# Performance work log

Measured on AMD Instinct MI355X. Metric: run time of the kernel, lower is better.

The kernel has to match this reference:

```python
import jax, jax.numpy as jnp
import numpy as np

NEMBEDS = 512
EMBED_DIM = 64


def setup_inputs() -> dict:
    key = jax.random.key(0)
    k1, k2 = jax.random.split(key)
    z_e = jax.random.normal(k1, (32, EMBED_DIM, 64, 64), dtype=jnp.float32)
    codebook = jax.random.uniform(
        k2, (NEMBEDS, EMBED_DIM), dtype=jnp.float32,
        minval=-1.0 / NEMBEDS, maxval=1.0 / NEMBEDS)
    return {"z_e": z_e, "codebook": codebook}


def reference(z_e, codebook):
    # NCHW -> NHWC, flatten spatial+batch into tokens
    z = jnp.transpose(z_e, (0, 2, 3, 1))          # [B,H,W,D]
    B, H, W, D = z.shape
    flat = z.reshape(-1, D)                        # [N,D]
    # squared L2 distances (argmin of ||.||_2 == argmin of ||.||_2^2)
    # expanded form avoids the [N,K,D] broadcast intermediate
    d2 = (jnp.sum(flat * flat, axis=-1, keepdims=True)
          - 2.0 * flat @ codebook.T
          + jnp.sum(codebook * codebook, axis=-1))  # [N,K]
    inds = jnp.argmin(d2, axis=1)                   # [N]
    # direct gather == one-hot matmul lookup
    z_q = codebook[inds].reshape(B, H, W, D)        # [B,H,W,D]
    # commitment + codebook loss, per-batch mean over H,W,D
    sg = jax.lax.stop_gradient
    vq_loss = (jnp.mean((sg(z) - z_q) ** 2, axis=(1, 2, 3))
               + 0.25 * jnp.mean((z - sg(z_q)) ** 2, axis=(1, 2, 3)))  # [B]
    # straight-through estimator
    z_q_st = z + sg(z_q - z)
    out = jnp.transpose(z_q_st, (0, 3, 1, 2))       # back to NCHW
    return out, vq_loss, inds[:, None]
```

## Files before the change

kernel.cpp:

```cpp
#include <hip/hip_runtime.h>

#define NEMB 512
#define DIM 64
#define NB 32
#define HW 4096
#define NTOK (NB * HW)
#define TPB 256
#define TOKBLK 256
#define BLOCKS (NTOK / TOKBLK)

typedef float f32x16 __attribute__((ext_vector_type(16)));
typedef short bf16x8 __attribute__((ext_vector_type(8)));

#define WS_PART 0
#define WS_SUMC 512
#define WS_CMAXP 1024
#define WS_SCMAXP 1032
#define WS_CH 1040

__device__ __forceinline__ unsigned short f2bf(float f) {
    unsigned u = __float_as_uint(f);
    unsigned r = u + 0x7FFFu + ((u >> 16) & 1u);
    return (unsigned short)(r >> 16);
}

__global__ void vq_prep(const float* __restrict__ cb, float* __restrict__ ws)
{
    const int tid = threadIdx.x;
    const int k   = blockIdx.x * 64 + tid;

    float sc_v;
    {
#pragma clang fp contract(off)
        float s = 0.f;
#pragma unroll
        for (int d = 0; d < DIM; ++d) {
            float v = cb[k * DIM + d];
            float p = v * v;
            s = s + p;
        }
        sc_v = s;
        ws[WS_SUMC + k] = s;
    }

    float cmax_t = 0.f;
    uint4* chf = (uint4*)(ws + WS_CH);
    const int ct  = k >> 5;
    const int col = k & 31;
#pragma unroll
    for (int bd = 0; bd < 8; ++bd) {
        unsigned wd[4];
#pragma unroll
        for (int q = 0; q < 4; ++q) {
            float v0 = cb[k * DIM + 8 * bd + 2 * q];
            float v1 = cb[k * DIM + 8 * bd + 2 * q + 1];
            cmax_t = fmaxf(cmax_t, fmaxf(fabsf(v0), fabsf(v1)));
            wd[q] = (unsigned)f2bf(v0) | ((unsigned)f2bf(v1) << 16);
        }
        chf[(ct * 8 + bd) * 32 + col] = make_uint4(wd[0], wd[1], wd[2], wd[3]);
    }

    float cm = cmax_t, sm = sc_v;
#pragma unroll
    for (int off = 32; off; off >>= 1) {
        cm = fmaxf(cm, __shfl_xor(cm, off));
        sm = fmaxf(sm, __shfl_xor(sm, off));
    }
    if (tid == 0) {
        ws[WS_CMAXP  + blockIdx.x] = cm;
        ws[WS_SCMAXP + blockIdx.x] = sm;
    }
}

__global__ __launch_bounds__(TPB, 2)
void vq_main(const float* __restrict__ z_e, const float* __restrict__ cb,
             const float* __restrict__ ws, float* __restrict__ out,
             float* __restrict__ loss_part, float* __restrict__ inds_out)
{
    __shared__ float sumc_s[NEMB];
    __shared__ float red_s[TPB];
    __shared__ float sc2[2];

    const int tid  = threadIdx.x;
    const int gid  = blockIdx.x;
    const int b    = gid >> 4;
    const int base = (gid & 15) * TOKBLK;
    const int l    = tid & 63;
    const int col  = l & 31;
    const int half = l >> 5;

    sumc_s[tid]       = ws[WS_SUMC + tid];
    sumc_s[tid + TPB] = ws[WS_SUMC + tid + TPB];
    if (tid == 0) {
        float cm = ws[WS_CMAXP], sm = ws[WS_SCMAXP];
#pragma unroll
        for (int i = 1; i < 8; ++i) {
            cm = fmaxf(cm, ws[WS_CMAXP + i]);
            sm = fmaxf(sm, ws[WS_SCMAXP + i]);
        }
        sc2[0] = cm; sc2[1] = sm;
    }

    const float* zb = z_e + (size_t)b * DIM * HW;
    const int hwme = base + tid;
    float z[DIM];
    float sumz;
    {
#pragma clang fp contract(off)
        sumz = 0.f;
#pragma unroll
        for (int d = 0; d < DIM; ++d) {
            float v = zb[(size_t)d * HW + hwme];
            z[d] = v;
            float p = v * v;
            sumz = sumz + p;
        }
    }
    float l1own = 0.f, szown = 0.f;
#pragma unroll
    for (int d = 0; d < DIM; ++d) {
        l1own += fabsf(z[d]);
        szown = fmaf(z[d], z[d], szown);
    }

    uint4 bzh[2][4];
#pragma unroll
    for (int tt = 0; tt < 2; ++tt) {
        int src = tt * 32 + col;
#pragma unroll
        for (int ks = 0; ks < 4; ++ks) {
            unsigned hh[8];
#pragma unroll
            for (int j = 0; j < 8; ++j) {
                float vlo = __shfl(z[16 * ks + j],     src);
                float vhi = __shfl(z[16 * ks + 8 + j], src);
                hh[j] = f2bf(half ? vhi : vlo);
            }
            bzh[tt][ks] = make_uint4(hh[0] | (hh[1] << 16), hh[2] | (hh[3] << 16),
                                     hh[4] | (hh[5] << 16), hh[6] | (hh[7] << 16));
        }
    }
    float L1[2], SZ[2];
#pragma unroll
    for (int tt = 0; tt < 2; ++tt) {
        L1[tt] = __shfl(l1own, tt * 32 + col);
        SZ[tt] = __shfl(szown, tt * 32 + col);
    }
    __syncthreads();

    const float cmax = sc2[0], scmax = sc2[1];
    float gapd[2];
#pragma unroll
    for (int tt = 0; tt < 2; ++tt)
        gapd[tt] = 1.6e-2f * cmax * L1[tt] + 0.5f * scmax + 1.2e-7f * SZ[tt] + 1e-6f;

    const uint4* chf = (const uint4*)(ws + WS_CH);
    unsigned mask0[8], mask1[8];
#pragma unroll
    for (int i = 0; i < 8; ++i) { mask0[i] = 0u; mask1[i] = 0u; }
    float runm[2] = {-3.402823466e38f, -3.402823466e38f};

    for (int ct = 0; ct < 16; ++ct) {
        bf16x8 ah[4];
#pragma unroll
        for (int ks = 0; ks < 4; ++ks) {
            uint4 u1 = chf[(ct * 8 + 2 * ks + half) * 32 + col];
            ah[ks] = *(bf16x8*)&u1;
        }
#pragma unroll
        for (int tt = 0; tt < 2; ++tt) {
            f32x16 acc = {0.f, 0.f, 0.f, 0.f, 0.f, 0.f, 0.f, 0.f,
                          0.f, 0.f, 0.f, 0.f, 0.f, 0.f, 0.f, 0.f};
#pragma unroll
            for (int ks = 0; ks < 4; ++ks)
                acc = __builtin_amdgcn_mfma_f32_32x32x16_bf16(ah[ks], *(bf16x8*)&bzh[tt][ks], acc, 0, 0, 0);
            float m = acc[0];
#pragma unroll
            for (int r = 1; r < 16; ++r) m = fmaxf(m, acc[r]);
            float rm = fmaxf(tt == 0 ? runm[0] : runm[1], m);
            if (tt == 0) runm[0] = rm; else runm[1] = rm;
            float thr = rm - (tt == 0 ? gapd[0] : gapd[1]);
            unsigned bits = 0;
#pragma unroll
            for (int r = 0; r < 16; ++r)
                bits |= (acc[r] >= thr) ? (1u << r) : 0u;
            unsigned sh = bits << ((ct & 1) * 16);
            if (tt == 0) mask0[ct >> 1] |= sh; else mask1[ct >> 1] |= sh;
        }
    }

    unsigned om[8], xm[8];
#pragma unroll
    for (int i = 0; i < 8; ++i) {
        om[i] = half ? mask1[i] : mask0[i];
        xm[i] = __shfl_xor(half ? mask0[i] : mask1[i], 32);
    }

    float best = 3.402823466e38f;
    int bk = 0;
    for (int ct = 0; ct < 16; ++ct) {
        unsigned A = (om[ct >> 1] >> ((ct & 1) * 16)) & 0xFFFFu;
        unsigned B = (xm[ct >> 1] >> ((ct & 1) * 16)) & 0xFFFFu;
        unsigned wo = ((A & 0xFu)) | (((A >> 4) & 0xFu) << 8) |
                      (((A >> 8) & 0xFu) << 16) | (((A >> 12) & 0xFu) << 24);
        unsigned wx = ((B & 0xFu)) | (((B >> 4) & 0xFu) << 8) |
                      (((B >> 8) & 0xFu) << 16) | (((B >> 12) & 0xFu) << 24);
        unsigned wc = half ? ((wo << 4) | wx) : (wo | (wx << 4));
        while (wc) {
            int kk = __builtin_ctz(wc);
            wc &= wc - 1;
            int k = 32 * ct + kk;
            const float4* c4 = (const float4*)(cb + (size_t)k * DIM);
            float a0 = 0.f;
#pragma unroll
            for (int g = 0; g < DIM / 4; ++g) {
                float4 u = c4[g];
                a0 = fmaf(z[4 * g + 0], u.x, a0);
                a0 = fmaf(z[4 * g + 1], u.y, a0);
                a0 = fmaf(z[4 * g + 2], u.z, a0);
                a0 = fmaf(z[4 * g + 3], u.w, a0);
            }
            float d2 = (sumz - 2.0f * a0) + sumc_s[k];
            if (d2 < best) { best = d2; bk = k; }
        }
    }

    inds_out[(size_t)gid * TOKBLK + tid] = (float)bk;
    float* ob = out + (size_t)b * DIM * HW;
    float lsum = 0.f;
    const float4* q4 = (const float4*)(cb + (size_t)bk * DIM);
    {
#pragma clang fp contract(off)
#pragma unroll
        for (int g = 0; g < DIM / 4; ++g) {
            float4 qq = q4[g];
            float qv[4] = {qq.x, qq.y, qq.z, qq.w};
#pragma unroll
            for (int j = 0; j < 4; ++j) {
                int d = g * 4 + j;
                float t1 = qv[j] - z[d];
                ob[(size_t)d * HW + hwme] = z[d] + t1;
                float p = t1 * t1;
                lsum = lsum + p;
            }
        }
    }

    __syncthreads();
    red_s[tid] = lsum;
    __syncthreads();
#pragma unroll
    for (int s = 128; s > 0; s >>= 1) {
        if (tid < s) red_s[tid] = red_s[tid] + red_s[tid + s];
        __syncthreads();
    }
    if (tid == 0) loss_part[gid] = red_s[0];
}

__global__ void vq_loss_final(const float* __restrict__ part,
                              float* __restrict__ loss_out)
{
    int b = threadIdx.x;
    if (b < NB) {
        float s = 0.f;
        for (int i = 0; i < 16; ++i)
            s = s + part[b * 16 + i];
        float m = s * (1.0f / (HW * DIM));
        loss_out[b] = m + 0.25f * m;
    }
}

extern "C" void kernel_launch(void* const* d_in, const int* in_sizes, int n_in,
                              void* d_out, int out_size, void* d_ws, size_t ws_size,
                              hipStream_t stream)
{
    const float* z_e = (const float*)d_in[0];
    const float* cb  = (const float*)d_in[1];

    float* out  = (float*)d_out;
    float* loss = out + (size_t)NB * DIM * HW;
    float* inds = loss + NB;
    float* ws   = (float*)d_ws;

    vq_prep<<<8, 64, 0, stream>>>(cb, ws);
    vq_main<<<BLOCKS, TPB, 0, stream>>>(z_e, cb, ws, out, ws + WS_PART, inds);
    vq_loss_final<<<1, 64, 0, stream>>>(ws + WS_PART, loss);
}
```

Before: 96.35 us.

## Split codebook search across two thread groups per token block and merge

Doubles the block size so each token is handled by two threads, each scanning half of the codebook with MFMA candidate filtering and exact rescoring. Each thread keeps a per-half best distance and index. These are merged through shared memory, and the first 256 threads then write outputs and the loss. The aim is more wavefronts per CU and a shorter serial loop over codebook tiles. In exchange, both groups load the same z values, and the tighter register budget under launch_bounds(512,2) risks spilling the 64-float z array.

```diff
diff --git a/kernel.cpp b/kernel.cpp
--- a/kernel.cpp
+++ b/kernel.cpp
@@ -5,7 +5,7 @@
 #define NB 32
 #define HW 4096
 #define NTOK (NB * HW)
-#define TPB 256
+#define TPB 512
 #define TOKBLK 256
 #define BLOCKS (NTOK / TOKBLK)
 
@@ -78,7 +78,9 @@
              float* __restrict__ loss_part, float* __restrict__ inds_out)
 {
     __shared__ float sumc_s[NEMB];
-    __shared__ float red_s[TPB];
+    __shared__ float bestL[TPB];
+    __shared__ int   bkL[TPB];
+    __shared__ float red_s[TOKBLK];
     __shared__ float sc2[2];
 
     const int tid  = threadIdx.x;
@@ -88,9 +90,10 @@
     const int l    = tid & 63;
     const int col  = l & 31;
     const int half = l >> 5;
-
-    sumc_s[tid]       = ws[WS_SUMC + tid];
-    sumc_s[tid + TPB] = ws[WS_SUMC + tid + TPB];
+    const int grp  = tid >> 8;
+    const int tok_in_blk = tid & 255;
+
+    sumc_s[tid & 511] = ws[WS_SUMC + (tid & 511)];
     if (tid == 0) {
         float cm = ws[WS_CMAXP], sm = ws[WS_SCMAXP];
 #pragma unroll
@@ -102,7 +105,7 @@
     }
 
     const float* zb = z_e + (size_t)b * DIM * HW;
-    const int hwme = base + tid;
+    const int hwme = base + tok_in_blk;
     float z[DIM];
     float sumz;
     {
@@ -155,16 +158,17 @@
         gapd[tt] = 1.6e-2f * cmax * L1[tt] + 0.5f * scmax + 1.2e-7f * SZ[tt] + 1e-6f;
 
     const uint4* chf = (const uint4*)(ws + WS_CH);
-    unsigned mask0[8], mask1[8];
-#pragma unroll
-    for (int i = 0; i < 8; ++i) { mask0[i] = 0u; mask1[i] = 0u; }
+    unsigned mask0[4], mask1[4];
+#pragma unroll
+    for (int i = 0; i < 4; ++i) { mask0[i] = 0u; mask1[i] = 0u; }
     float runm[2] = {-3.402823466e38f, -3.402823466e38f};
 
-    for (int ct = 0; ct < 16; ++ct) {
+    for (int ctl = 0; ctl < 8; ++ctl) {
+        const int ctg = (grp << 3) | ctl;
         bf16x8 ah[4];
 #pragma unroll
         for (int ks = 0; ks < 4; ++ks) {
-            uint4 u1 = chf[(ct * 8 + 2 * ks + half) * 32 + col];
+            uint4 u1 = chf[(ctg * 8 + 2 * ks + half) * 32 + col];
             ah[ks] = *(bf16x8*)&u1;
         }
 #pragma unroll
@@ -184,23 +188,23 @@
 #pragma unroll
             for (int r = 0; r < 16; ++r)
                 bits |= (acc[r] >= thr) ? (1u << r) : 0u;
-            unsigned sh = bits << ((ct & 1) * 16);
-            if (tt == 0) mask0[ct >> 1] |= sh; else mask1[ct >> 1] |= sh;
-        }
-    }
-
-    unsigned om[8], xm[8];
-#pragma unroll
-    for (int i = 0; i < 8; ++i) {
+            unsigned sh = bits << ((ctl & 1) * 16);
+            if (tt == 0) mask0[ctl >> 1] |= sh; else mask1[ctl >> 1] |= sh;
+        }
+    }
+
+    unsigned om[4], xm[4];
+#pragma unroll
+    for (int i = 0; i < 4; ++i) {
         om[i] = half ? mask1[i] : mask0[i];
         xm[i] = __shfl_xor(half ? mask0[i] : mask1[i], 32);
     }
 
     float best = 3.402823466e38f;
-    int bk = 0;
-    for (int ct = 0; ct < 16; ++ct) {
-        unsigned A = (om[ct >> 1] >> ((ct & 1) * 16)) & 0xFFFFu;
-        unsigned B = (xm[ct >> 1] >> ((ct & 1) * 16)) & 0xFFFFu;
+    int bk = grp << 8;
+    for (int ctl = 0; ctl < 8; ++ctl) {
+        unsigned A = (om[ctl >> 1] >> ((ctl & 1) * 16)) & 0xFFFFu;
+        unsigned B = (xm[ctl >> 1] >> ((ctl & 1) * 16)) & 0xFFFFu;
         unsigned wo = ((A & 0xFu)) | (((A >> 4) & 0xFu) << 8) |
                       (((A >> 8) & 0xFu) << 16) | (((A >> 12) & 0xFu) << 24);
         unsigned wx = ((B & 0xFu)) | (((B >> 4) & 0xFu) << 8) |
@@ -209,7 +213,7 @@
         while (wc) {
             int kk = __builtin_ctz(wc);
             wc &= wc - 1;
-            int k = 32 * ct + kk;
+            int k = ((grp << 3) | ctl) * 32 + kk;
             const float4* c4 = (const float4*)(cb + (size_t)k * DIM);
             float a0 = 0.f;
 #pragma unroll
@@ -225,29 +229,40 @@
         }
     }
 
-    inds_out[(size_t)gid * TOKBLK + tid] = (float)bk;
-    float* ob = out + (size_t)b * DIM * HW;
+    bestL[tid] = best;
+    bkL[tid]   = bk;
+    __syncthreads();
+
     float lsum = 0.f;
-    const float4* q4 = (const float4*)(cb + (size_t)bk * DIM);
-    {
+    if (tid < 256) {
+        float bA = bestL[tid];
+        float bB = bestL[tid + 256];
+        int   mk = (bB < bA) ? bkL[tid + 256] : bkL[tid];
+
+        inds_out[(size_t)gid * TOKBLK + tid] = (float)mk;
+
+        float* ob = out + (size_t)b * DIM * HW;
+        const float4* q4 = (const float4*)(cb + (size_t)mk * DIM);
+        {
 #pragma clang fp contract(off)
 #pragma unroll
-        for (int g = 0; g < DIM / 4; ++g) {
-            float4 qq = q4[g];
-            float qv[4] = {qq.x, qq.y, qq.z, qq.w};
-#pragma unroll
-            for (int j = 0; j < 4; ++j) {
-                int d = g * 4 + j;
-                float t1 = qv[j] - z[d];
-                ob[(size_t)d * HW + hwme] = z[d] + t1;
-                float p = t1 * t1;
-                lsum = lsum + p;
+            for (int g = 0; g < DIM / 4; ++g) {
+                float4 qq = q4[g];
+                float qv[4] = {qq.x, qq.y, qq.z, qq.w};
+#pragma unroll
+                for (int j = 0; j < 4; ++j) {
+                    int d = g * 4 + j;
+                    float t1 = qv[j] - z[d];
+                    ob[(size_t)d * HW + hwme] = z[d] + t1;
+                    float p = t1 * t1;
+                    lsum = lsum + p;
+                }
             }
         }
     }
 
     __syncthreads();
-    red_s[tid] = lsum;
+    if (tid < 256) red_s[tid] = lsum;
     __syncthreads();
 #pragma unroll
     for (int s = 128; s > 0; s >>= 1) {
```

New measurement: 118.9 us. 23.4% more time.
